# Kernel optimization log

Hardware: AMD Instinct MI355X
Metric: run time of the kernel (lower is better)

Reference implementation:

```python
import jax, jax.numpy as jnp
import numpy as np

BN_EPS = 1e-5


def sparsemax(z):
    # z: [B, D]; sparse projection onto the simplex along last axis.
    D = z.shape[-1]
    z_sorted = jnp.flip(jnp.sort(z, axis=-1), axis=-1)          # descending
    cs = jnp.cumsum(z_sorted, axis=-1)                           # cumulative sums
    k = jnp.arange(1, D + 1, dtype=z.dtype)                      # 1..D
    support = (1.0 + k * z_sorted) > cs                          # support condition
    k_star = jnp.sum(support, axis=-1, keepdims=True)            # support size, int
    cs_k = jnp.take_along_axis(cs, k_star - 1, axis=-1)
    tau = (cs_k - 1.0) / k_star.astype(z.dtype)                  # threshold
    return jnp.maximum(z - tau, 0.0)


def setup_inputs() -> dict:
    key = jax.random.key(0)
    k1, k2, k3 = jax.random.split(key, 3)
    B, D = 32768, 1024
    a = jax.random.normal(k1, (B, D), dtype=jnp.float32)
    p = jax.random.uniform(k2, (B, D), dtype=jnp.float32)        # prior scales in (0,1)
    W = jax.random.normal(k3, (D, D), dtype=jnp.float32) * (1.0 / np.sqrt(D))
    b = jnp.zeros((D,), dtype=jnp.float32)
    gamma = jnp.ones((D,), dtype=jnp.float32)
    beta = jnp.zeros((D,), dtype=jnp.float32)
    return {"a": a, "p": p, "W": W, "b": b, "gamma": gamma, "beta": beta}


def reference(a, p, W, b, gamma, beta):
    # Linear: a @ W^T + b  (torch nn.Linear convention)
    h = jnp.einsum("bd,ed->be", a, W) + b
    # BatchNorm1d (training mode: batch stats, biased variance)
    mean = jnp.mean(h, axis=0)
    var = jnp.mean(jnp.square(h - mean), axis=0)
    h = (h - mean) * jax.lax.rsqrt(var + BN_EPS) * gamma + beta
    # Prior scaling, then sparsemax -> attention mask
    mask = sparsemax(p * h)
    return mask
```

## Files before the change

kernel.cpp:

```cpp
#include <hip/hip_runtime.h>
#include <hip/hip_fp16.h>
#include <stdint.h>

typedef _Float16 f16x8 __attribute__((ext_vector_type(8)));
typedef _Float16 f16x4 __attribute__((ext_vector_type(4)));
typedef float f32x4 __attribute__((ext_vector_type(4)));

#define BM 128
#define BN 128
#define BK 64

__device__ __forceinline__ void async_copy16(const void* g, void* l) {
  __builtin_amdgcn_global_load_lds(
      (__attribute__((address_space(1))) void*)(g),
      (__attribute__((address_space(3))) void*)(l),
      16, 0, 0);
}

__global__ __launch_bounds__(256) void cvt_f32_f16(const float* __restrict__ in,
                                                   _Float16* __restrict__ out,
                                                   size_t n) {
  size_t i = ((size_t)blockIdx.x * 256 + threadIdx.x) * 8;
  if (i + 8 > n) return;
  float4 u = *(const float4*)(in + i);
  float4 v = *(const float4*)(in + i + 4);
  f16x8 h;
  h[0] = (_Float16)u.x; h[1] = (_Float16)u.y; h[2] = (_Float16)u.z; h[3] = (_Float16)u.w;
  h[4] = (_Float16)v.x; h[5] = (_Float16)v.y; h[6] = (_Float16)v.z; h[7] = (_Float16)v.w;
  *(f16x8*)(out + i) = h;
}

template <bool H16>
__global__ __launch_bounds__(256) void gemm_direct(const _Float16* __restrict__ Ah,
                                                   const _Float16* __restrict__ Wh,
                                                   const float* __restrict__ bias,
                                                   void* __restrict__ Hout,
                                                   float* __restrict__ psum,
                                                   float* __restrict__ psumsq,
                                                   int M, int N, int K) {
  __shared__ __attribute__((aligned(16))) _Float16 lsA[BM * BK];
  __shared__ __attribute__((aligned(16))) _Float16 lsB[BN * BK];

  const int tid  = threadIdx.x;
  const int wave = tid >> 6;
  const int lane = tid & 63;
  const int wrow = (wave >> 1) * 64;
  const int wcol = (wave & 1) * 64;
  const int l16  = lane & 15;
  const int quad = lane >> 4;

  const int nx = gridDim.x;
  const int li = blockIdx.y * nx + blockIdx.x;
  const int xcd = li & 7;
  const int jj  = li >> 3;
  const int bnT = jj % nx;
  const int bmT = xcd + (jj / nx) * 8;
  const int bm = bmT * BM;
  const int bn = bnT * BN;

  f32x4 acc[4][4];
#pragma unroll
  for (int i = 0; i < 4; ++i)
#pragma unroll
    for (int j = 0; j < 4; ++j) acc[i][j] = (f32x4){0.f, 0.f, 0.f, 0.f};

  for (int k0 = 0; k0 < K; k0 += BK) {
#pragma unroll
    for (int i = 0; i < 4; ++i) {
      const int basechunk = i * 256 + wave * 64;
      const int g   = basechunk + lane;
      const int row = g >> 3;
      const int kc  = ((g & 7) ^ (row & 7)) << 3;
      async_copy16(Ah + (size_t)(bm + row) * K + k0 + kc, &lsA[basechunk * 8]);
      async_copy16(Wh + (size_t)(bn + row) * K + k0 + kc, &lsB[basechunk * 8]);
    }
    __syncthreads();

#pragma unroll
    for (int kk = 0; kk < BK; kk += 32) {
      f16x8 af[4], bf[4];
#pragma unroll
      for (int i = 0; i < 4; ++i) {
        const int r = wrow + i * 16 + l16;
        const int col = ((kk >> 3) + quad) ^ (l16 & 7);
        af[i] = *(const f16x8*)&lsA[r * 64 + col * 8];
      }
#pragma unroll
      for (int j = 0; j < 4; ++j) {
        const int r = wcol + j * 16 + l16;
        const int col = ((kk >> 3) + quad) ^ (l16 & 7);
        bf[j] = *(const f16x8*)&lsB[r * 64 + col * 8];
      }
#pragma unroll
      for (int i = 0; i < 4; ++i)
#pragma unroll
        for (int j = 0; j < 4; ++j)
          acc[i][j] = __builtin_amdgcn_mfma_f32_16x16x32_f16(af[i], bf[j], acc[i][j], 0, 0, 0);
    }
    __syncthreads();
  }

  const int PS = (M >> 7) * 2;
#pragma unroll
  for (int j = 0; j < 4; ++j) {
    const int c = bn + wcol + j * 16 + l16;
    const float bv = bias[c];
    float s = 0.f, s2 = 0.f;
#pragma unroll
    for (int i = 0; i < 4; ++i) {
      const int r = bm + wrow + i * 16 + quad * 4;
      f32x4 v = acc[i][j];
#pragma unroll
      for (int rr = 0; rr < 4; ++rr) {
        float val = v[rr] + bv;
        if constexpr (H16) {
          ((_Float16*)Hout)[(size_t)(r + rr) * N + c] = (_Float16)val;
        } else {
          ((float*)Hout)[(size_t)(r + rr) * N + c] = val;
        }
        s += val;
        s2 += val * val;
      }
    }
    s  += __shfl_xor(s, 16, 64);  s  += __shfl_xor(s, 32, 64);
    s2 += __shfl_xor(s2, 16, 64); s2 += __shfl_xor(s2, 32, 64);
    if (quad == 0) {
      const size_t slot = (size_t)c * PS + bmT * 2 + (wave >> 1);
      psum[slot] = s;
      psumsq[slot] = s2;
    }
  }
}

__global__ __launch_bounds__(256) void gemm_fallback(const float* __restrict__ Af,
                                                     const float* __restrict__ Wf,
                                                     const float* __restrict__ bias,
                                                     float* __restrict__ C,
                                                     float* __restrict__ sum,
                                                     float* __restrict__ sumsq,
                                                     int M, int N, int K) {
  __shared__ __attribute__((aligned(16))) _Float16 lsA[BM * BK];
  __shared__ __attribute__((aligned(16))) _Float16 lsB[BN * BK];
  const int tid  = threadIdx.x;
  const int wave = tid >> 6;
  const int lane = tid & 63;
  const int wrow = (wave >> 1) * 64;
  const int wcol = (wave & 1) * 64;
  const int l16  = lane & 15;
  const int quad = lane >> 4;
  const int bm = blockIdx.y * BM;
  const int bn = blockIdx.x * BN;

  f32x4 acc[4][4];
#pragma unroll
  for (int i = 0; i < 4; ++i)
#pragma unroll
    for (int j = 0; j < 4; ++j) acc[i][j] = (f32x4){0.f, 0.f, 0.f, 0.f};

  for (int k0 = 0; k0 < K; k0 += BK) {
#pragma unroll
    for (int i = 0; i < 4; ++i) {
      const int g   = i * 256 + tid;
      const int row = g >> 3;
      const int kc  = ((g & 7) ^ (row & 7)) << 3;
      {
        const float* src = Af + (size_t)(bm + row) * K + k0 + kc;
        float4 u = *(const float4*)src;
        float4 v = *(const float4*)(src + 4);
        f16x8 h;
        h[0] = (_Float16)u.x; h[1] = (_Float16)u.y; h[2] = (_Float16)u.z; h[3] = (_Float16)u.w;
        h[4] = (_Float16)v.x; h[5] = (_Float16)v.y; h[6] = (_Float16)v.z; h[7] = (_Float16)v.w;
        *(f16x8*)&lsA[g * 8] = h;
      }
      {
        const float* src = Wf + (size_t)(bn + row) * K + k0 + kc;
        float4 u = *(const float4*)src;
        float4 v = *(const float4*)(src + 4);
        f16x8 h;
        h[0] = (_Float16)u.x; h[1] = (_Float16)u.y; h[2] = (_Float16)u.z; h[3] = (_Float16)u.w;
        h[4] = (_Float16)v.x; h[5] = (_Float16)v.y; h[6] = (_Float16)v.z; h[7] = (_Float16)v.w;
        *(f16x8*)&lsB[g * 8] = h;
      }
    }
    __syncthreads();
#pragma unroll
    for (int kk = 0; kk < BK; kk += 32) {
      f16x8 af[4], bf[4];
#pragma unroll
      for (int i = 0; i < 4; ++i) {
        const int r = wrow + i * 16 + l16;
        const int col = ((kk >> 3) + quad) ^ (l16 & 7);
        af[i] = *(const f16x8*)&lsA[r * 64 + col * 8];
      }
#pragma unroll
      for (int j = 0; j < 4; ++j) {
        const int r = wcol + j * 16 + l16;
        const int col = ((kk >> 3) + quad) ^ (l16 & 7);
        bf[j] = *(const f16x8*)&lsB[r * 64 + col * 8];
      }
#pragma unroll
      for (int i = 0; i < 4; ++i)
#pragma unroll
        for (int j = 0; j < 4; ++j)
          acc[i][j] = __builtin_amdgcn_mfma_f32_16x16x32_f16(af[i], bf[j], acc[i][j], 0, 0, 0);
    }
    __syncthreads();
  }

#pragma unroll
  for (int j = 0; j < 4; ++j) {
    const int c = bn + wcol + j * 16 + l16;
    const float bv = bias[c];
    float s = 0.f, s2 = 0.f;
#pragma unroll
    for (int i = 0; i < 4; ++i) {
      const int r = bm + wrow + i * 16 + quad * 4;
      float* Cp = C + (size_t)r * N + c;
      f32x4 v = acc[i][j];
#pragma unroll
      for (int rr = 0; rr < 4; ++rr) {
        float val = v[rr] + bv;
        Cp[(size_t)rr * N] = val;
        s += val;
        s2 += val * val;
      }
    }
    s  += __shfl_xor(s, 16, 64);  s  += __shfl_xor(s, 32, 64);
    s2 += __shfl_xor(s2, 16, 64); s2 += __shfl_xor(s2, 32, 64);
    if (quad == 0) {
      atomicAdd(&sum[c], s);
      atomicAdd(&sumsq[c], s2);
    }
  }
}

__global__ __launch_bounds__(256) void bn_finalize_direct(const float* __restrict__ psum,
                                                          const float* __restrict__ psumsq,
                                                          const float* __restrict__ gamma,
                                                          const float* __restrict__ beta,
                                                          float* __restrict__ scale,
                                                          float* __restrict__ shift,
                                                          float invB, int PS) {
  const int wave = threadIdx.x >> 6;
  const int lane = threadIdx.x & 63;
  const int c = blockIdx.x * 4 + wave;
  const f32x4* ps = (const f32x4*)(psum + (size_t)c * PS);
  const f32x4* pq = (const f32x4*)(psumsq + (size_t)c * PS);
  float s = 0.f, q = 0.f;
  for (int k = lane; k < (PS >> 2); k += 64) {
    f32x4 v = ps[k]; s += v[0] + v[1] + v[2] + v[3];
    f32x4 w = pq[k]; q += w[0] + w[1] + w[2] + w[3];
  }
#pragma unroll
  for (int o = 32; o > 0; o >>= 1) {
    s += __shfl_xor(s, o, 64);
    q += __shfl_xor(q, o, 64);
  }
  if (lane == 0) {
    float mean = s * invB;
    float var  = q * invB - mean * mean;
    float rstd = rsqrtf(var + 1e-5f);
    float sc = rstd * gamma[c];
    scale[c] = sc;
    shift[c] = beta[c] - mean * sc;
  }
}

__global__ __launch_bounds__(256) void bn_finalize(const float* __restrict__ sum,
                                                   const float* __restrict__ sumsq,
                                                   const float* __restrict__ gamma,
                                                   const float* __restrict__ beta,
                                                   float* __restrict__ scale,
                                                   float* __restrict__ shift,
                                                   float invB) {
  const int c = blockIdx.x * 256 + threadIdx.x;
  float mean = sum[c] * invB;
  float var  = sumsq[c] * invB - mean * mean;
  float rstd = rsqrtf(var + 1e-5f);
  float sc = rstd * gamma[c];
  scale[c] = sc;
  shift[c] = beta[c] - mean * sc;
}

template <bool H16>
__global__ __launch_bounds__(256) void bn_sparsemax(const void* H,
                                                    const float* __restrict__ P,
                                                    const float* __restrict__ scale,
                                                    const float* __restrict__ shift,
                                                    float* out, int D) {
  const int wave = threadIdx.x >> 6;
  const int lane = threadIdx.x & 63;
  const int row = blockIdx.x * 4 + wave;
  const size_t rowoff = (size_t)row * D;

  const f32x4* P4 = (const f32x4*)(P + rowoff);
  const f32x4* SC = (const f32x4*)scale;
  const f32x4* SH = (const f32x4*)shift;

  f32x4 z[4];
  float tot = 0.f;
#pragma unroll
  for (int j = 0; j < 4; ++j) {
    const int idx = j * 64 + lane;
    f32x4 hv;
    if constexpr (H16) {
      f16x4 h4 = ((const f16x4*)((const _Float16*)H + rowoff))[idx];
      hv[0] = (float)h4[0]; hv[1] = (float)h4[1]; hv[2] = (float)h4[2]; hv[3] = (float)h4[3];
    } else {
      hv = ((const f32x4*)((const float*)H + rowoff))[idx];
    }
    f32x4 zz = P4[idx] * (hv * SC[idx] + SH[idx]);
    z[j] = zz;
    tot += zz[0] + zz[1] + zz[2] + zz[3];
  }
#pragma unroll
  for (int o = 32; o > 0; o >>= 1) tot += __shfl_xor(tot, o, 64);

  float tau = (tot - 1.0f) / (float)D;
  float kprev = -1.0f;
  for (int it = 0; it < 64; ++it) {
    float s = 0.f, kf = 0.f;
#pragma unroll
    for (int j = 0; j < 4; ++j)
#pragma unroll
      for (int c = 0; c < 4; ++c) {
        float zz = z[j][c];
        if (zz > tau) { s += zz; kf += 1.0f; }
      }
#pragma unroll
    for (int o = 32; o > 0; o >>= 1) {
      s  += __shfl_xor(s, o, 64);
      kf += __shfl_xor(kf, o, 64);
    }
    tau = (s - 1.0f) / kf;
    if (kf == kprev) break;
    kprev = kf;
  }

  f32x4* O4 = (f32x4*)(out + rowoff);
#pragma unroll
  for (int j = 0; j < 4; ++j) {
    const int idx = j * 64 + lane;
    f32x4 o;
#pragma unroll
    for (int c = 0; c < 4; ++c) o[c] = fmaxf(z[j][c] - tau, 0.f);
    O4[idx] = o;
  }
}

extern "C" void kernel_launch(void* const* d_in, const int* in_sizes, int n_in,
                              void* d_out, int out_size, void* d_ws, size_t ws_size,
                              hipStream_t stream) {
  const float* a     = (const float*)d_in[0];
  const float* p     = (const float*)d_in[1];
  const float* W     = (const float*)d_in[2];
  const float* b     = (const float*)d_in[3];
  const float* gamma = (const float*)d_in[4];
  const float* beta  = (const float*)d_in[5];
  float* out = (float*)d_out;

  const int D = in_sizes[3];
  const int Brows = in_sizes[0] / D;
  const int K = D, N = D;
  const size_t na = (size_t)Brows * D;
  const size_t nw = (size_t)D * D;
  const int PS = (Brows / BM) * 2;

  const size_t statsB = (size_t)D * PS * sizeof(float);
  float* psum   = (float*)d_ws;
  float* psumsq = (float*)((char*)d_ws + statsB);
  float* wscale = (float*)((char*)d_ws + 2 * statsB);
  float* wshift = wscale + D;
  const size_t off_Ah = 2 * statsB + 16384;
  _Float16* Ah = (_Float16*)((char*)d_ws + off_Ah);
  _Float16* Wh = Ah + na;
  _Float16* Hh = Wh + nw;
  const size_t need1 = off_Ah + (na + nw) * sizeof(_Float16);
  const size_t need2 = need1 + na * sizeof(_Float16);

  if (ws_size >= need1) {
    cvt_f32_f16<<<dim3((unsigned)(na / 8 / 256)), 256, 0, stream>>>(a, Ah, na);
    cvt_f32_f16<<<dim3((unsigned)(nw / 8 / 256)), 256, 0, stream>>>(W, Wh, nw);
    const bool h16 = ws_size >= need2;
    if (h16) {
      gemm_direct<true><<<dim3(N / BN, Brows / BM), 256, 0, stream>>>(
          Ah, Wh, b, Hh, psum, psumsq, Brows, N, K);
    } else {
      gemm_direct<false><<<dim3(N / BN, Brows / BM), 256, 0, stream>>>(
          Ah, Wh, b, out, psum, psumsq, Brows, N, K);
    }
    bn_finalize_direct<<<dim3(D / 4), 256, 0, stream>>>(psum, psumsq, gamma, beta,
                                                        wscale, wshift,
                                                        1.0f / (float)Brows, PS);
    if (h16) {
      bn_sparsemax<true><<<dim3(Brows / 4), 256, 0, stream>>>(Hh, p, wscale, wshift, out, D);
    } else {
      bn_sparsemax<false><<<dim3(Brows / 4), 256, 0, stream>>>(out, p, wscale, wshift, out, D);
    }
  } else {
    float* wsum   = (float*)d_ws;
    float* wsumsq = wsum + D;
    float* fscale = wsum + 2 * D;
    float* fshift = wsum + 3 * D;
    hipMemsetAsync(d_ws, 0, 2 * D * sizeof(float), stream);
    gemm_fallback<<<dim3(N / BN, Brows / BM), 256, 0, stream>>>(
        a, W, b, out, wsum, wsumsq, Brows, N, K);
    bn_finalize<<<dim3(D / 256), 256, 0, stream>>>(wsum, wsumsq, gamma, beta, fscale, fshift,
                                                   1.0f / (float)Brows);
    bn_sparsemax<false><<<dim3(Brows / 4), 256, 0, stream>>>(out, p, fscale, fshift, out, D);
  }
}
```

Measured before the change: 437.5 us.

## Interleave row pairs in fp16 H and process two rows per sparsemax wave

```diff
diff --git a/kernel.cpp b/kernel.cpp
--- a/kernel.cpp
+++ b/kernel.cpp
@@ -3,7 +3,7 @@
 #include <stdint.h>
 
 typedef _Float16 f16x8 __attribute__((ext_vector_type(8)));
-typedef _Float16 f16x4 __attribute__((ext_vector_type(4)));
+typedef _Float16 f16x2 __attribute__((ext_vector_type(2)));
 typedef float f32x4 __attribute__((ext_vector_type(4)));
 
 #define BM 128
@@ -100,7 +100,6 @@
     __syncthreads();
   }
 
-  const int PS = (M >> 7) * 2;
 #pragma unroll
   for (int j = 0; j < 4; ++j) {
     const int c = bn + wcol + j * 16 + l16;
@@ -110,22 +109,23 @@
     for (int i = 0; i < 4; ++i) {
       const int r = bm + wrow + i * 16 + quad * 4;
       f32x4 v = acc[i][j];
-#pragma unroll
-      for (int rr = 0; rr < 4; ++rr) {
-        float val = v[rr] + bv;
-        if constexpr (H16) {
-          ((_Float16*)Hout)[(size_t)(r + rr) * N + c] = (_Float16)val;
-        } else {
-          ((float*)Hout)[(size_t)(r + rr) * N + c] = val;
-        }
-        s += val;
-        s2 += val * val;
+      const float v0 = v[0] + bv, v1 = v[1] + bv, v2 = v[2] + bv, v3 = v[3] + bv;
+      s += v0 + v1 + v2 + v3;
+      s2 += v0 * v0 + v1 * v1 + v2 * v2 + v3 * v3;
+      if constexpr (H16) {
+        f16x2* H2 = (f16x2*)Hout;
+        const size_t d0 = (size_t)(r >> 1) * N + c;
+        H2[d0]     = (f16x2){(_Float16)v0, (_Float16)v1};
+        H2[d0 + N] = (f16x2){(_Float16)v2, (_Float16)v3};
+      } else {
+        float* Cp = (float*)Hout + (size_t)r * N + c;
+        Cp[0] = v0; Cp[(size_t)N] = v1; Cp[2 * (size_t)N] = v2; Cp[3 * (size_t)N] = v3;
       }
     }
     s  += __shfl_xor(s, 16, 64);  s  += __shfl_xor(s, 32, 64);
     s2 += __shfl_xor(s2, 16, 64); s2 += __shfl_xor(s2, 32, 64);
     if (quad == 0) {
-      const size_t slot = (size_t)c * PS + bmT * 2 + (wave >> 1);
+      const size_t slot = (size_t)(bmT * 2 + (wave >> 1)) * N + c;
       psum[slot] = s;
       psumsq[slot] = s2;
     }
@@ -234,36 +234,28 @@
   }
 }
 
-__global__ __launch_bounds__(256) void bn_finalize_direct(const float* __restrict__ psum,
-                                                          const float* __restrict__ psumsq,
-                                                          const float* __restrict__ gamma,
-                                                          const float* __restrict__ beta,
-                                                          float* __restrict__ scale,
-                                                          float* __restrict__ shift,
-                                                          float invB, int PS) {
-  const int wave = threadIdx.x >> 6;
-  const int lane = threadIdx.x & 63;
-  const int c = blockIdx.x * 4 + wave;
-  const f32x4* ps = (const f32x4*)(psum + (size_t)c * PS);
-  const f32x4* pq = (const f32x4*)(psumsq + (size_t)c * PS);
+__global__ __launch_bounds__(256) void bn_finalize_sc(const float* __restrict__ psum,
+                                                      const float* __restrict__ psumsq,
+                                                      const float* __restrict__ gamma,
+                                                      const float* __restrict__ beta,
+                                                      float* __restrict__ scale,
+                                                      float* __restrict__ shift,
+                                                      float invB, int S, int D) {
+  const int c = blockIdx.x * 256 + threadIdx.x;
   float s = 0.f, q = 0.f;
-  for (int k = lane; k < (PS >> 2); k += 64) {
-    f32x4 v = ps[k]; s += v[0] + v[1] + v[2] + v[3];
-    f32x4 w = pq[k]; q += w[0] + w[1] + w[2] + w[3];
-  }
-#pragma unroll
-  for (int o = 32; o > 0; o >>= 1) {
-    s += __shfl_xor(s, o, 64);
-    q += __shfl_xor(q, o, 64);
-  }
-  if (lane == 0) {
-    float mean = s * invB;
-    float var  = q * invB - mean * mean;
-    float rstd = rsqrtf(var + 1e-5f);
-    float sc = rstd * gamma[c];
-    scale[c] = sc;
-    shift[c] = beta[c] - mean * sc;
-  }
+  for (int s0 = 0; s0 < S; s0 += 8) {
+#pragma unroll
+    for (int u = 0; u < 8; ++u) {
+      s += psum[(size_t)(s0 + u) * D + c];
+      q += psumsq[(size_t)(s0 + u) * D + c];
+    }
+  }
+  float mean = s * invB;
+  float var  = q * invB - mean * mean;
+  float rstd = rsqrtf(var + 1e-5f);
+  float sc = rstd * gamma[c];
+  scale[c] = sc;
+  shift[c] = beta[c] - mean * sc;
 }
 
 __global__ __launch_bounds__(256) void bn_finalize(const float* __restrict__ sum,
@@ -282,17 +274,94 @@
   shift[c] = beta[c] - mean * sc;
 }
 
-template <bool H16>
-__global__ __launch_bounds__(256) void bn_sparsemax(const void* H,
-                                                    const float* __restrict__ P,
-                                                    const float* __restrict__ scale,
-                                                    const float* __restrict__ shift,
-                                                    float* out, int D) {
+__global__ __launch_bounds__(256) void bn_sparsemax_pair(const _Float16* __restrict__ H2,
+                                                         const float* __restrict__ P,
+                                                         const float* __restrict__ scale,
+                                                         const float* __restrict__ shift,
+                                                         float* __restrict__ out, int D) {
+  const int wave = threadIdx.x >> 6;
+  const int lane = threadIdx.x & 63;
+  const int rp = blockIdx.x * 4 + wave;
+
+  const f16x8* Hc = (const f16x8*)(H2 + (size_t)rp * 2 * D);
+  const f32x4* P0 = (const f32x4*)(P + (size_t)(2 * rp) * D);
+  const f32x4* P1 = (const f32x4*)(P + (size_t)(2 * rp + 1) * D);
+  const f32x4* SC = (const f32x4*)scale;
+  const f32x4* SH = (const f32x4*)shift;
+
+  f32x4 z0[4], z1[4];
+  float tot0 = 0.f, tot1 = 0.f;
+#pragma unroll
+  for (int j = 0; j < 4; ++j) {
+    const int idx = j * 64 + lane;
+    f16x8 h = Hc[idx];
+    f32x4 h0 = {(float)h[0], (float)h[2], (float)h[4], (float)h[6]};
+    f32x4 h1 = {(float)h[1], (float)h[3], (float)h[5], (float)h[7]};
+    f32x4 sc = SC[idx], sh = SH[idx];
+    f32x4 a0 = P0[idx] * (h0 * sc + sh);
+    f32x4 a1 = P1[idx] * (h1 * sc + sh);
+    z0[j] = a0; z1[j] = a1;
+    tot0 += a0[0] + a0[1] + a0[2] + a0[3];
+    tot1 += a1[0] + a1[1] + a1[2] + a1[3];
+  }
+#pragma unroll
+  for (int o = 32; o > 0; o >>= 1) {
+    tot0 += __shfl_xor(tot0, o, 64);
+    tot1 += __shfl_xor(tot1, o, 64);
+  }
+
+  float tau0 = (tot0 - 1.0f) / (float)D;
+  float tau1 = (tot1 - 1.0f) / (float)D;
+  float k0p = -1.0f, k1p = -1.0f;
+  for (int it = 0; it < 64; ++it) {
+    float s0 = 0.f, k0 = 0.f, s1 = 0.f, k1 = 0.f;
+#pragma unroll
+    for (int j = 0; j < 4; ++j)
+#pragma unroll
+      for (int c = 0; c < 4; ++c) {
+        float a = z0[j][c], bv = z1[j][c];
+        if (a > tau0)  { s0 += a;  k0 += 1.0f; }
+        if (bv > tau1) { s1 += bv; k1 += 1.0f; }
+      }
+#pragma unroll
+    for (int o = 32; o > 0; o >>= 1) {
+      s0 += __shfl_xor(s0, o, 64);
+      k0 += __shfl_xor(k0, o, 64);
+      s1 += __shfl_xor(s1, o, 64);
+      k1 += __shfl_xor(k1, o, 64);
+    }
+    tau0 = (s0 - 1.0f) / k0;
+    tau1 = (s1 - 1.0f) / k1;
+    if (k0 == k0p && k1 == k1p) break;
+    k0p = k0; k1p = k1;
+  }
+
+  f32x4* O0 = (f32x4*)(out + (size_t)(2 * rp) * D);
+  f32x4* O1 = (f32x4*)(out + (size_t)(2 * rp + 1) * D);
+#pragma unroll
+  for (int j = 0; j < 4; ++j) {
+    const int idx = j * 64 + lane;
+    f32x4 o0, o1;
+#pragma unroll
+    for (int c = 0; c < 4; ++c) {
+      o0[c] = fmaxf(z0[j][c] - tau0, 0.f);
+      o1[c] = fmaxf(z1[j][c] - tau1, 0.f);
+    }
+    O0[idx] = o0;
+    O1[idx] = o1;
+  }
+}
+
+__global__ __launch_bounds__(256) void bn_sparsemax_f32(const float* __restrict__ H,
+                                                        const float* __restrict__ P,
+                                                        const float* __restrict__ scale,
+                                                        const float* __restrict__ shift,
+                                                        float* __restrict__ out, int D) {
   const int wave = threadIdx.x >> 6;
   const int lane = threadIdx.x & 63;
   const int row = blockIdx.x * 4 + wave;
   const size_t rowoff = (size_t)row * D;
-
+  const f32x4* H4 = (const f32x4*)(H + rowoff);
   const f32x4* P4 = (const f32x4*)(P + rowoff);
   const f32x4* SC = (const f32x4*)scale;
   const f32x4* SH = (const f32x4*)shift;
@@ -302,14 +371,7 @@
 #pragma unroll
   for (int j = 0; j < 4; ++j) {
     const int idx = j * 64 + lane;
-    f32x4 hv;
-    if constexpr (H16) {
-      f16x4 h4 = ((const f16x4*)((const _Float16*)H + rowoff))[idx];
-      hv[0] = (float)h4[0]; hv[1] = (float)h4[1]; hv[2] = (float)h4[2]; hv[3] = (float)h4[3];
-    } else {
-      hv = ((const f32x4*)((const float*)H + rowoff))[idx];
-    }
-    f32x4 zz = P4[idx] * (hv * SC[idx] + SH[idx]);
+    f32x4 zz = P4[idx] * (H4[idx] * SC[idx] + SH[idx]);
     z[j] = zz;
     tot += zz[0] + zz[1] + zz[2] + zz[3];
   }
@@ -364,9 +426,9 @@
   const int K = D, N = D;
   const size_t na = (size_t)Brows * D;
   const size_t nw = (size_t)D * D;
-  const int PS = (Brows / BM) * 2;
-
-  const size_t statsB = (size_t)D * PS * sizeof(float);
+  const int S = (Brows / BM) * 2;
+
+  const size_t statsB = (size_t)D * S * sizeof(float);
   float* psum   = (float*)d_ws;
   float* psumsq = (float*)((char*)d_ws + statsB);
   float* wscale = (float*)((char*)d_ws + 2 * statsB);
@@ -374,7 +436,7 @@
   const size_t off_Ah = 2 * statsB + 16384;
   _Float16* Ah = (_Float16*)((char*)d_ws + off_Ah);
   _Float16* Wh = Ah + na;
-  _Float16* Hh = Wh + nw;
+  _Float16* H2 = Wh + nw;
   const size_t need1 = off_Ah + (na + nw) * sizeof(_Float16);
   const size_t need2 = need1 + na * sizeof(_Float16);
 
@@ -384,18 +446,18 @@
     const bool h16 = ws_size >= need2;
     if (h16) {
       gemm_direct<true><<<dim3(N / BN, Brows / BM), 256, 0, stream>>>(
-          Ah, Wh, b, Hh, psum, psumsq, Brows, N, K);
+          Ah, Wh, b, H2, psum, psumsq, Brows, N, K);
     } else {
       gemm_direct<false><<<dim3(N / BN, Brows / BM), 256, 0, stream>>>(
           Ah, Wh, b, out, psum, psumsq, Brows, N, K);
     }
-    bn_finalize_direct<<<dim3(D / 4), 256, 0, stream>>>(psum, psumsq, gamma, beta,
-                                                        wscale, wshift,
-                                                        1.0f / (float)Brows, PS);
+    bn_finalize_sc<<<dim3(D / 256), 256, 0, stream>>>(psum, psumsq, gamma, beta,
+                                                      wscale, wshift,
+                                                      1.0f / (float)Brows, S, D);
     if (h16) {
-      bn_sparsemax<true><<<dim3(Brows / 4), 256, 0, stream>>>(Hh, p, wscale, wshift, out, D);
+      bn_sparsemax_pair<<<dim3(Brows / 8), 256, 0, stream>>>(H2, p, wscale, wshift, out, D);
     } else {
-      bn_sparsemax<false><<<dim3(Brows / 4), 256, 0, stream>>>(out, p, wscale, wshift, out, D);
+      bn_sparsemax_f32<<<dim3(Brows / 4), 256, 0, stream>>>(out, p, wscale, wshift, out, D);
     }
   } else {
     float* wsum   = (float*)d_ws;
@@ -407,6 +469,6 @@
         a, W, b, out, wsum, wsumsq, Brows, N, K);
     bn_finalize<<<dim3(D / 256), 256, 0, stream>>>(wsum, wsumsq, gamma, beta, fscale, fshift,
                                                    1.0f / (float)Brows);
-    bn_sparsemax<false><<<dim3(Brows / 4), 256, 0, stream>>>(out, p, fscale, fshift, out, D);
-  }
-}
+    bn_sparsemax_f32<<<dim3(Brows / 4), 256, 0, stream>>>(out, p, fscale, fshift, out, D);
+  }
+}
```

Result: no change. 445.8 us (+1.9%).
